# Kernel optimization log

Measured on AMD Instinct MI355X. Metric: run time of the kernel, lower is better.

Reference implementation:

```python
import jax, jax.numpy as jnp
import numpy as np

N_NODES = 100000
N_EDGES = 1600000
IN_FEATS = 512
OUT_FEATS = 256


def setup_inputs() -> dict:
    key = jax.random.key(0)
    k1, k2, k3, k4, k5 = jax.random.split(key, 5)
    feat = jax.random.normal(k1, (N_NODES, IN_FEATS), dtype=jnp.float32)
    W = jax.random.normal(k2, (OUT_FEATS, IN_FEATS), dtype=jnp.float32) * (1.0 / np.sqrt(IN_FEATS))
    b = jax.random.normal(k3, (OUT_FEATS,), dtype=jnp.float32) * 0.01
    src = jax.random.randint(k4, (N_EDGES,), 0, N_NODES, dtype=jnp.int32)
    dst = jax.random.randint(k5, (N_EDGES,), 0, N_NODES, dtype=jnp.int32)
    return {"feat": feat, "W": W, "b": b, "src": src, "dst": dst}


def reference(feat, W, b, src, dst):
    # Linear projection: h = feat @ W^T + b   -> [N, out_feats]
    h = jnp.einsum('nf,of->no', feat, W) + b
    # DGL update_all(copy_src, sum): for each edge (s, d), message = h[s],
    # reduce = sum over incoming edges at each destination node.
    # Nodes with no in-edges get zeros (DGL sum-reduce default).
    msgs = h[src]  # [E, out_feats] gather
    h_out = jax.ops.segment_sum(msgs, dst, num_segments=N_NODES)  # [N, out_feats]
    return h_out
```

## Files before the change

### kernel.cpp

```cpp
#include <hip/hip_runtime.h>
#include <hip/hip_bf16.h>
#include <stdint.h>

#define N_NODES 100000
#define IN_F    512
#define OUT_F   256
#define N_EDGES 1600000

typedef __attribute__((ext_vector_type(4))) float f32x4;
typedef __attribute__((ext_vector_type(8))) short bf16x8;
typedef __attribute__((ext_vector_type(8))) uint16_t u16x8;
typedef __attribute__((ext_vector_type(4))) uint32_t u32x4;

#define BM 128
#define BK 32
#define KT_TILES (IN_F / BK)
#define WFRAG_KT_STRIDE (16 * 16 * 32)
#define EPS 66

#define NBUCK 196
#define BCAP  9216
#define SC_EDGES 8192
#define NBLK_SC ((N_EDGES + SC_EDGES - 1) / SC_EDGES)

__device__ __forceinline__ float bf2f(uint16_t u) {
    union { uint32_t i; float f; } c; c.i = ((uint32_t)u) << 16; return c.f;
}
__device__ __forceinline__ uint16_t f2bf(float f) {
    union { float f; uint32_t i; } c; c.f = f;
    uint32_t x = c.i;
    return (uint16_t)((x + 0x7FFFu + ((x >> 16) & 1u)) >> 16);
}
__device__ __forceinline__ uint32_t cvt_pk_bf16(float a, float b) {
    uint32_t r;
    asm("v_cvt_pk_bf16_f32 %0, %1, %2" : "=v"(r) : "v"(a), "v"(b));
    return r;
}
__device__ __forceinline__ void gload_lds16(const float* g, float* l) {
    __builtin_amdgcn_global_load_lds(
        (const __attribute__((address_space(1))) void*)g,
        (__attribute__((address_space(3))) void*)l, 16, 0, 0);
}
#define SYNC_VM(N) do {                                        \
    asm volatile("s_waitcnt vmcnt(" #N ")" ::: "memory");      \
    __builtin_amdgcn_s_barrier();                              \
} while (0)

__global__ __launch_bounds__(256) void w_frag_kernel(
    const float* __restrict__ W, uint16_t* __restrict__ w_frag)
{
    const int gid = blockIdx.x * 256 + threadIdx.x;
    if (gid >= 16384) return;
    const int kg = gid & 3, lrow = (gid >> 2) & 15, cg = (gid >> 6) & 15, kt = gid >> 10;
    const float* s = W + (size_t)(cg * 16 + lrow) * IN_F + kt * 32 + kg * 8;
    const f32x4 v0 = *(const f32x4*)s;
    const f32x4 v1 = *(const f32x4*)(s + 4);
    u32x4 c;
    c[0] = cvt_pk_bf16(v0[0], v0[1]);
    c[1] = cvt_pk_bf16(v0[2], v0[3]);
    c[2] = cvt_pk_bf16(v1[0], v1[1]);
    c[3] = cvt_pk_bf16(v1[2], v1[3]);
    *(u32x4*)(w_frag + (size_t)gid * 8) = c;
}

__global__ __launch_bounds__(512) void gcn_gemm_kernel(
    const float* __restrict__ feat, const uint16_t* __restrict__ w_frag,
    const float* __restrict__ bias, uint16_t* __restrict__ h)
{
    __shared__ __align__(16) char smem_raw[3 * BM * BK * 4];
    float (*At)[BM][BK] = (float (*)[BM][BK])smem_raw;

    const int m0 = blockIdx.x * BM;

    const int t    = threadIdx.x;
    const int wid  = t >> 6;
    const int lane = t & 63;
    const int wr   = wid >> 2, wc = wid & 3;
    const int lrow = lane & 15;
    const int kg   = lane >> 4;

    f32x4 acc[4][4] = {};

    const int r8 = lane >> 3;
    const int sp = lane & 7;
    const int sc = sp ^ r8;
    const float* gsrc[2];
    #pragma unroll
    for (int i = 0; i < 2; ++i) {
        int grow = m0 + wid * 16 + i * 8 + r8;
        if (grow > N_NODES - 1) grow = N_NODES - 1;
        gsrc[i] = feat + (size_t)grow * IN_F + sc * 4;
    }

#define STAGE(KT, BUF)                                                     \
    do {                                                                   \
        gload_lds16(gsrc[0] + (KT) * BK, &At[BUF][wid * 16][0]);           \
        gload_lds16(gsrc[1] + (KT) * BK, &At[BUF][wid * 16 + 8][0]);       \
    } while (0)

    const uint16_t* wfp[4];
    #pragma unroll
    for (int n = 0; n < 4; ++n) {
        const int cg = wc * 4 + n;
        wfp[n] = w_frag + ((size_t)cg * 16 + lrow) * 32 + kg * 8;
    }

    bf16x8 bfr[2][4];

    #pragma unroll
    for (int n = 0; n < 4; ++n) bfr[0][n] = *(const bf16x8*)(wfp[n]);
    STAGE(0, 0);
    STAGE(1, 1);
    SYNC_VM(0);

    const int p0 = (2 * kg) ^ (lrow & 7);
    const int p1 = p0 ^ 1;

    #pragma unroll
    for (int kt = 0; kt < KT_TILES; ++kt) {
        const int cur = kt % 3;
        if (kt + 1 < KT_TILES) {
            #pragma unroll
            for (int n = 0; n < 4; ++n)
                bfr[(kt + 1) & 1][n] =
                    *(const bf16x8*)(wfp[n] + (size_t)(kt + 1) * WFRAG_KT_STRIDE);
        }
        if (kt + 2 < KT_TILES) STAGE(kt + 2, (kt + 2) % 3);

        bf16x8 af[4];
        #pragma unroll
        for (int m = 0; m < 4; ++m) {
            const int row = wr * 64 + m * 16 + lrow;
            const f32x4 v0 = *(const f32x4*)&At[cur][row][p0 * 4];
            const f32x4 v1 = *(const f32x4*)&At[cur][row][p1 * 4];
            union { bf16x8 v; uint32_t u[4]; } c_;
            c_.u[0] = cvt_pk_bf16(v0[0], v0[1]);
            c_.u[1] = cvt_pk_bf16(v0[2], v0[3]);
            c_.u[2] = cvt_pk_bf16(v1[0], v1[1]);
            c_.u[3] = cvt_pk_bf16(v1[2], v1[3]);
            af[m] = c_.v;
        }
        #pragma unroll
        for (int m = 0; m < 4; ++m)
            #pragma unroll
            for (int n = 0; n < 4; ++n)
                acc[m][n] = __builtin_amdgcn_mfma_f32_16x16x32_bf16(
                    af[m], bfr[kt & 1][n], acc[m][n], 0, 0, 0);

        if (kt <= KT_TILES - 3)       SYNC_VM(6);
        else if (kt == KT_TILES - 2)  SYNC_VM(4);
    }
#undef STAGE

    __syncthreads();

    uint16_t* ep = (uint16_t*)smem_raw;
    const int wbase = wid * (16 * EPS);
    float bv[4];
    #pragma unroll
    for (int n = 0; n < 4; ++n) bv[n] = bias[wc * 64 + n * 16 + lrow];

    #pragma unroll
    for (int m = 0; m < 4; ++m) {
        #pragma unroll
        for (int n = 0; n < 4; ++n)
            #pragma unroll
            for (int j = 0; j < 4; ++j)
                ep[wbase + (kg * 4 + j) * EPS + n * 16 + lrow] = f2bf(acc[m][n][j] + bv[n]);
        __syncthreads();
        #pragma unroll
        for (int g = 0; g < 4; ++g) {
            const int r16  = g * 4 + (lane >> 4);
            const int cidx = (lane & 15) * 4;
            const int ib = wbase + r16 * EPS + cidx;
            uint2 v;
            v.x = *(const uint32_t*)&ep[ib];
            v.y = *(const uint32_t*)&ep[ib + 2];
            const int row = m0 + wr * 64 + m * 16 + r16;
            if (row < N_NODES)
                *(uint2*)(h + (size_t)row * OUT_F + wc * 64 + cidx) = v;
        }
        __syncthreads();
    }
}

__global__ void bucket_init_kernel(int* __restrict__ bucket_cursor)
{
    const int i = threadIdx.x;
    if (i < NBUCK) bucket_cursor[i] = i * BCAP;
}

__global__ __launch_bounds__(256) void bucket_scatter_kernel(
    const int* __restrict__ src, const int* __restrict__ dst,
    int* __restrict__ bucket_cursor, uint32_t* __restrict__ pairs)
{
    __shared__ int bh[NBUCK];
    __shared__ int bbase[NBUCK];
    for (int i = threadIdx.x; i < NBUCK; i += 256) bh[i] = 0;
    __syncthreads();
    const int base = blockIdx.x * SC_EDGES;
    uint32_t pk[SC_EDGES / 256];
    int      bk[SC_EDGES / 256];
    #pragma unroll
    for (int k = 0; k < SC_EDGES / 256; ++k) {
        const int e = base + k * 256 + threadIdx.x;
        if (e < N_EDGES) {
            const int d = dst[e], s = src[e];
            bk[k] = d >> 9;
            pk[k] = ((uint32_t)s << 9) | (uint32_t)(d & 511);
            atomicAdd(&bh[bk[k]], 1);
        } else {
            bk[k] = -1; pk[k] = 0;
        }
    }
    __syncthreads();
    for (int i = threadIdx.x; i < NBUCK; i += 256) {
        const int c = bh[i];
        bbase[i] = c ? atomicAdd(&bucket_cursor[i], c) : 0;
        bh[i] = 0;
    }
    __syncthreads();
    #pragma unroll
    for (int k = 0; k < SC_EDGES / 256; ++k) {
        if (bk[k] >= 0) {
            const int r = atomicAdd(&bh[bk[k]], 1);
            pairs[bbase[bk[k]] + r] = pk[k];
        }
    }
}

__global__ __launch_bounds__(256) void bucket_sort_kernel(
    const uint32_t* __restrict__ pairs, const int* __restrict__ bucket_cursor,
    int* __restrict__ start, int* __restrict__ deg, int* __restrict__ csr_src)
{
    __shared__ int hist[512];
    __shared__ int tsum[256];
    const int b = blockIdx.x;
    const int t = threadIdx.x;
    const int ebeg = b * BCAP;
    const int eend = bucket_cursor[b];
    hist[t] = 0; hist[t + 256] = 0;
    __syncthreads();
    for (int i = ebeg + t; i < eend; i += 256)
        atomicAdd(&hist[pairs[i] & 511], 1);
    __syncthreads();
    const int c0 = hist[2 * t], c1 = hist[2 * t + 1];
    int x = c0 + c1;
    tsum[t] = x; __syncthreads();
    for (int off = 1; off < 256; off <<= 1) {
        const int y = (t >= off) ? tsum[t - off] : 0;
        __syncthreads();
        x += y; tsum[t] = x;
        __syncthreads();
    }
    const int ex = x - (c0 + c1);
    __syncthreads();
    hist[2 * t] = ex;
    hist[2 * t + 1] = ex + c0;
    const int nb0 = b << 9;
    if (nb0 + 2 * t < N_NODES) {
        start[nb0 + 2 * t] = ebeg + ex;
        deg[nb0 + 2 * t]   = c0;
    }
    if (nb0 + 2 * t + 1 < N_NODES) {
        start[nb0 + 2 * t + 1] = ebeg + ex + c0;
        deg[nb0 + 2 * t + 1]   = c1;
    }
    __syncthreads();
    for (int i = ebeg + t; i < eend; i += 256) {
        const uint32_t p = pairs[i];
        const int pos = ebeg + atomicAdd(&hist[p & 511], 1);
        csr_src[pos] = (int)(p >> 9);
    }
}

__global__ __launch_bounds__(256) void gcn_gather_kernel(
    const uint16_t* __restrict__ h, const int* __restrict__ start,
    const int* __restrict__ deg, const int* __restrict__ csr_src,
    float* __restrict__ out)
{
    const int n = blockIdx.x * 4 + (threadIdx.x >> 6);
    if (n >= N_NODES) return;
    const int lane = threadIdx.x & 63;
    const int half = lane >> 5;
    const int hl   = lane & 31;
    const int beg = start[n];
    const int end = beg + deg[n];

    float a[8] = {0.f, 0.f, 0.f, 0.f, 0.f, 0.f, 0.f, 0.f};

    int j = beg + half;
    for (; j + 2 < end; j += 4) {
        const int s0 = csr_src[j];
        const int s1 = csr_src[j + 2];
        const u16x8 v0 = *(const u16x8*)(h + (size_t)s0 * OUT_F + hl * 8);
        const u16x8 v1 = *(const u16x8*)(h + (size_t)s1 * OUT_F + hl * 8);
        #pragma unroll
        for (int i = 0; i < 8; ++i) a[i] += bf2f(v0[i]);
        #pragma unroll
        for (int i = 0; i < 8; ++i) a[i] += bf2f(v1[i]);
    }
    if (j < end) {
        const int s0 = csr_src[j];
        const u16x8 v0 = *(const u16x8*)(h + (size_t)s0 * OUT_F + hl * 8);
        #pragma unroll
        for (int i = 0; i < 8; ++i) a[i] += bf2f(v0[i]);
    }

    #pragma unroll
    for (int i = 0; i < 8; ++i) a[i] += __shfl_xor(a[i], 32, 64);

    if (half == 0) {
        f32x4 o0, o1;
        o0[0] = a[0]; o0[1] = a[1]; o0[2] = a[2]; o0[3] = a[3];
        o1[0] = a[4]; o1[1] = a[5]; o1[2] = a[6]; o1[3] = a[7];
        float* op = out + (size_t)n * OUT_F + hl * 8;
        *(f32x4*)op = o0;
        *(f32x4*)(op + 4) = o1;
    }
}

__global__ __launch_bounds__(256) void gcn_scatter_kernel(
    const uint16_t* __restrict__ h, const int* __restrict__ src,
    const int* __restrict__ dst, float* __restrict__ out)
{
    const int e = (blockIdx.x << 2) | (threadIdx.x >> 6);
    if (e >= N_EDGES) return;
    const int lane = threadIdx.x & 63;
    const int s = src[e];
    const int d = dst[e];
    const ushort4 v = *((const ushort4*)(h + (size_t)s * OUT_F) + lane);
    float* op = out + (size_t)d * OUT_F + (lane << 2);
    unsafeAtomicAdd(op + 0, bf2f(v.x));
    unsafeAtomicAdd(op + 1, bf2f(v.y));
    unsafeAtomicAdd(op + 2, bf2f(v.z));
    unsafeAtomicAdd(op + 3, bf2f(v.w));
}

static inline size_t align256(size_t x) { return (x + 255) & ~(size_t)255; }

extern "C" void kernel_launch(void* const* d_in, const int* in_sizes, int n_in,
                              void* d_out, int out_size, void* d_ws, size_t ws_size,
                              hipStream_t stream) {
    const float* feat = (const float*)d_in[0];
    const float* W    = (const float*)d_in[1];
    const float* bias = (const float*)d_in[2];
    const int*   src  = (const int*)d_in[3];
    const int*   dst  = (const int*)d_in[4];
    float*       out  = (float*)d_out;

    char* ws = (char*)d_ws;

    size_t off = 0;
    uint16_t* h       = (uint16_t*)(ws + off); off = align256(off + (size_t)N_NODES * OUT_F * 2);
    uint16_t* w_frag  = (uint16_t*)(ws + off); off = align256(off + (size_t)OUT_F * IN_F * 2);
    int* start        = (int*)(ws + off);      off = align256(off + (size_t)N_NODES * 4);
    int* deg          = (int*)(ws + off);      off = align256(off + (size_t)N_NODES * 4);
    int* bucket_cursor= (int*)(ws + off);      off = align256(off + (size_t)NBUCK * 4);
    uint32_t* pairs   = (uint32_t*)(ws + off); off = align256(off + (size_t)NBUCK * BCAP * 4);
    int* csr_src      = (int*)(ws + off);      off = align256(off + (size_t)NBUCK * BCAP * 4);
    const bool bucket_ok = (off <= ws_size);

    const int mtiles = (N_NODES + BM - 1) / BM;

    w_frag_kernel<<<64, 256, 0, stream>>>(W, w_frag);
    gcn_gemm_kernel<<<mtiles, 512, 0, stream>>>(feat, w_frag, bias, h);

    if (bucket_ok) {
        bucket_init_kernel<<<1, 256, 0, stream>>>(bucket_cursor);
        bucket_scatter_kernel<<<NBLK_SC, 256, 0, stream>>>(src, dst, bucket_cursor, pairs);
        bucket_sort_kernel<<<NBUCK, 256, 0, stream>>>(pairs, bucket_cursor, start, deg, csr_src);
        gcn_gather_kernel<<<(N_NODES + 3) / 4, 256, 0, stream>>>(h, start, deg, csr_src, out);
    } else {
        hipMemsetAsync(out, 0, (size_t)out_size * sizeof(float), stream);
        gcn_scatter_kernel<<<(N_EDGES + 3) / 4, 256, 0, stream>>>(h, src, dst, out);
    }
}
```

Measured before the change: 245.9 us.

## Fuse edge bucket scatter into GEMM launch and use smaller buckets

Adds the edge bucketing work to the GEMM launch as extra blocks, so the scatter pass runs alongside the GEMM tiles and one launch is saved. Buckets now cover 256 destination nodes instead of 512, which gives 391 buckets and twice as many sort blocks. The sort kernel becomes simpler, with one node per thread and a separate cursor array. The risk is that scatter blocks compete with GEMM tiles for CUs, and the max bucket size of 4608 leaves less headroom for overflow.

Result: faster. 216.3 us (-12.1%).

```diff
diff --git a/kernel.cpp b/kernel.cpp
--- a/kernel.cpp
+++ b/kernel.cpp
@@ -17,9 +17,10 @@
 #define KT_TILES (IN_F / BK)
 #define WFRAG_KT_STRIDE (16 * 16 * 32)
 #define EPS 66
-
-#define NBUCK 196
-#define BCAP  9216
+#define MTILES ((N_NODES + BM - 1) / BM)
+
+#define NBUCK 391
+#define BCAP  4608
 #define SC_EDGES 8192
 #define NBLK_SC ((N_EDGES + SC_EDGES - 1) / SC_EDGES)
 
@@ -63,11 +64,58 @@
     *(u32x4*)(w_frag + (size_t)gid * 8) = c;
 }
 
-__global__ __launch_bounds__(512) void gcn_gemm_kernel(
+__global__ __launch_bounds__(512) void bucket_init_kernel(int* __restrict__ bucket_cursor)
+{
+    const int i = threadIdx.x;
+    if (i < NBUCK) bucket_cursor[i] = i * BCAP;
+}
+
+__global__ __launch_bounds__(512) void gemm_scatter_kernel(
     const float* __restrict__ feat, const uint16_t* __restrict__ w_frag,
-    const float* __restrict__ bias, uint16_t* __restrict__ h)
+    const float* __restrict__ bias, uint16_t* __restrict__ h,
+    const int* __restrict__ src, const int* __restrict__ dst,
+    int* __restrict__ bucket_cursor, uint32_t* __restrict__ pairs)
 {
     __shared__ __align__(16) char smem_raw[3 * BM * BK * 4];
+
+    if (blockIdx.x >= MTILES) {
+        int* bh    = (int*)smem_raw;
+        int* bbase = bh + NBUCK;
+        const int tid = threadIdx.x;
+        for (int i = tid; i < NBUCK; i += 512) bh[i] = 0;
+        __syncthreads();
+        const int base = (int)(blockIdx.x - MTILES) * SC_EDGES;
+        uint32_t pk[SC_EDGES / 512];
+        int      bk[SC_EDGES / 512];
+        #pragma unroll
+        for (int k = 0; k < SC_EDGES / 512; ++k) {
+            const int e = base + k * 512 + tid;
+            if (e < N_EDGES) {
+                const int d = dst[e], s = src[e];
+                bk[k] = d >> 8;
+                pk[k] = ((uint32_t)s << 8) | (uint32_t)(d & 255);
+                atomicAdd(&bh[bk[k]], 1);
+            } else {
+                bk[k] = -1; pk[k] = 0;
+            }
+        }
+        __syncthreads();
+        for (int i = tid; i < NBUCK; i += 512) {
+            const int c = bh[i];
+            bbase[i] = c ? atomicAdd(&bucket_cursor[i], c) : 0;
+            bh[i] = 0;
+        }
+        __syncthreads();
+        #pragma unroll
+        for (int k = 0; k < SC_EDGES / 512; ++k) {
+            if (bk[k] >= 0) {
+                const int r = atomicAdd(&bh[bk[k]], 1);
+                pairs[bbase[bk[k]] + r] = pk[k];
+            }
+        }
+        return;
+    }
+
     float (*At)[BM][BK] = (float (*)[BM][BK])smem_raw;
 
     const int m0 = blockIdx.x * BM;
@@ -184,68 +232,24 @@
     }
 }
 
-__global__ void bucket_init_kernel(int* __restrict__ bucket_cursor)
-{
-    const int i = threadIdx.x;
-    if (i < NBUCK) bucket_cursor[i] = i * BCAP;
-}
-
-__global__ __launch_bounds__(256) void bucket_scatter_kernel(
-    const int* __restrict__ src, const int* __restrict__ dst,
-    int* __restrict__ bucket_cursor, uint32_t* __restrict__ pairs)
-{
-    __shared__ int bh[NBUCK];
-    __shared__ int bbase[NBUCK];
-    for (int i = threadIdx.x; i < NBUCK; i += 256) bh[i] = 0;
-    __syncthreads();
-    const int base = blockIdx.x * SC_EDGES;
-    uint32_t pk[SC_EDGES / 256];
-    int      bk[SC_EDGES / 256];
-    #pragma unroll
-    for (int k = 0; k < SC_EDGES / 256; ++k) {
-        const int e = base + k * 256 + threadIdx.x;
-        if (e < N_EDGES) {
-            const int d = dst[e], s = src[e];
-            bk[k] = d >> 9;
-            pk[k] = ((uint32_t)s << 9) | (uint32_t)(d & 511);
-            atomicAdd(&bh[bk[k]], 1);
-        } else {
-            bk[k] = -1; pk[k] = 0;
-        }
-    }
-    __syncthreads();
-    for (int i = threadIdx.x; i < NBUCK; i += 256) {
-        const int c = bh[i];
-        bbase[i] = c ? atomicAdd(&bucket_cursor[i], c) : 0;
-        bh[i] = 0;
-    }
-    __syncthreads();
-    #pragma unroll
-    for (int k = 0; k < SC_EDGES / 256; ++k) {
-        if (bk[k] >= 0) {
-            const int r = atomicAdd(&bh[bk[k]], 1);
-            pairs[bbase[bk[k]] + r] = pk[k];
-        }
-    }
-}
-
 __global__ __launch_bounds__(256) void bucket_sort_kernel(
     const uint32_t* __restrict__ pairs, const int* __restrict__ bucket_cursor,
     int* __restrict__ start, int* __restrict__ deg, int* __restrict__ csr_src)
 {
-    __shared__ int hist[512];
+    __shared__ int hist[256];
+    __shared__ int cur[256];
     __shared__ int tsum[256];
     const int b = blockIdx.x;
     const int t = threadIdx.x;
     const int ebeg = b * BCAP;
     const int eend = bucket_cursor[b];
-    hist[t] = 0; hist[t + 256] = 0;
+    hist[t] = 0;
     __syncthreads();
     for (int i = ebeg + t; i < eend; i += 256)
-        atomicAdd(&hist[pairs[i] & 511], 1);
+        atomicAdd(&hist[pairs[i] & 255], 1);
     __syncthreads();
-    const int c0 = hist[2 * t], c1 = hist[2 * t + 1];
-    int x = c0 + c1;
+    const int c = hist[t];
+    int x = c;
     tsum[t] = x; __syncthreads();
     for (int off = 1; off < 256; off <<= 1) {
         const int y = (t >= off) ? tsum[t - off] : 0;
@@ -253,24 +257,18 @@
         x += y; tsum[t] = x;
         __syncthreads();
     }
-    const int ex = x - (c0 + c1);
-    __syncthreads();
-    hist[2 * t] = ex;
-    hist[2 * t + 1] = ex + c0;
-    const int nb0 = b << 9;
-    if (nb0 + 2 * t < N_NODES) {
-        start[nb0 + 2 * t] = ebeg + ex;
-        deg[nb0 + 2 * t]   = c0;
-    }
-    if (nb0 + 2 * t + 1 < N_NODES) {
-        start[nb0 + 2 * t + 1] = ebeg + ex + c0;
-        deg[nb0 + 2 * t + 1]   = c1;
-    }
+    const int ex = x - c;
+    const int node = (b << 8) + t;
+    if (node < N_NODES) {
+        start[node] = ebeg + ex;
+        deg[node]   = c;
+    }
+    cur[t] = ebeg + ex;
     __syncthreads();
     for (int i = ebeg + t; i < eend; i += 256) {
         const uint32_t p = pairs[i];
-        const int pos = ebeg + atomicAdd(&hist[p & 511], 1);
-        csr_src[pos] = (int)(p >> 9);
+        const int pos = atomicAdd(&cur[p & 255], 1);
+        csr_src[pos] = (int)(p >> 8);
     }
 }
 
@@ -361,17 +359,17 @@
     int* csr_src      = (int*)(ws + off);      off = align256(off + (size_t)NBUCK * BCAP * 4);
     const bool bucket_ok = (off <= ws_size);
 
-    const int mtiles = (N_NODES + BM - 1) / BM;
-
     w_frag_kernel<<<64, 256, 0, stream>>>(W, w_frag);
-    gcn_gemm_kernel<<<mtiles, 512, 0, stream>>>(feat, w_frag, bias, h);
 
     if (bucket_ok) {
-        bucket_init_kernel<<<1, 256, 0, stream>>>(bucket_cursor);
-        bucket_scatter_kernel<<<NBLK_SC, 256, 0, stream>>>(src, dst, bucket_cursor, pairs);
+        bucket_init_kernel<<<1, 512, 0, stream>>>(bucket_cursor);
+        gemm_scatter_kernel<<<MTILES + NBLK_SC, 512, 0, stream>>>(
+            feat, w_frag, bias, h, src, dst, bucket_cursor, pairs);
         bucket_sort_kernel<<<NBUCK, 256, 0, stream>>>(pairs, bucket_cursor, start, deg, csr_src);
         gcn_gather_kernel<<<(N_NODES + 3) / 4, 256, 0, stream>>>(h, start, deg, csr_src, out);
     } else {
+        gemm_scatter_kernel<<<MTILES, 512, 0, stream>>>(
+            feat, w_frag, bias, h, src, dst, (int*)d_ws, (uint32_t*)d_ws);
         hipMemsetAsync(out, 0, (size_t)out_size * sizeof(float), stream);
         gcn_scatter_kernel<<<(N_EDGES + 3) / 4, 256, 0, stream>>>(h, src, dst, out);
     }
```
